# Performance work log

Hardware: AMD Instinct MI355X
Metric: run time of the kernel (lower is better)

The kernel has to match this reference:

```python
import jax, jax.numpy as jnp
import numpy as np

N, F, E, H, C, K = 20000, 256, 400000, 4, 64, 3
NEG_SLOPE = 0.2


def setup_inputs() -> dict:
    key = jax.random.key(0)
    ks = jax.random.split(key, 13)
    x = jax.random.normal(ks[0], (N, F), jnp.float32)
    edge0 = jax.random.randint(ks[1], (2, E), 0, N)
    edge1 = jax.random.randint(ks[2], (2, E), 0, N)
    edge2 = jax.random.randint(ks[3], (2, E), 0, N)
    s = 1.0 / np.sqrt(F)
    Wl = jax.random.normal(ks[4], (F, H * C), jnp.float32) * s
    bl = jax.random.normal(ks[5], (H * C,), jnp.float32) * 0.02
    Wr = jax.random.normal(ks[6], (F, H * C), jnp.float32) * s
    br = jax.random.normal(ks[7], (H * C,), jnp.float32) * 0.02
    att = jax.random.normal(ks[8], (K, H, C), jnp.float32) * (1.0 / np.sqrt(C))
    bias_out = jax.random.normal(ks[9], (K, C), jnp.float32) * 0.02
    Wg = jax.random.normal(ks[10], (F, K), jnp.float32) * s
    bg = jax.random.normal(ks[11], (K,), jnp.float32) * 0.02
    return dict(x=x, edge0=edge0, edge1=edge1, edge2=edge2, Wl=Wl, bl=bl,
                Wr=Wr, br=br, att=att, bias_out=bias_out, Wg=Wg, bg=bg)


def _gatv2_hop(xl, xr, src, dst, att_h, b_h, num_nodes):
    # xl, xr: [N, H, C] projected features (shared across hops)
    # att_h: [H, C] hop-specific attention vector; b_h: [C] hop-specific bias
    e = jax.nn.leaky_relu(xl[src] + xr[dst], NEG_SLOPE)          # [E, H, C]
    s = jnp.einsum('ehc,hc->eh', e, att_h)                       # [E, H]
    smax = jax.ops.segment_max(s, dst, num_segments=num_nodes)   # [N, H]
    ex = jnp.exp(s - smax[dst])
    denom = jax.ops.segment_sum(ex, dst, num_segments=num_nodes)
    alpha = ex / denom[dst]                                      # softmax over in-edges of dst
    msg = jax.ops.segment_sum(alpha[:, :, None] * xl[src], dst, num_segments=num_nodes)  # [N,H,C]
    return msg.mean(axis=1) + b_h                                # concat=False -> mean heads


def reference(x, edge0, edge1, edge2, Wl, bl, Wr, br, att, bias_out, Wg, bg):
    num_nodes = x.shape[0]
    heads, ch = att.shape[1], att.shape[2]
    xl = (x @ Wl + bl).reshape(num_nodes, heads, ch)
    xr = (x @ Wr + br).reshape(num_nodes, heads, ch)
    # hop 0: add self-loops (add_self_loops=True only for k == 0)
    loop = jnp.arange(num_nodes, dtype=edge0.dtype)
    src0 = jnp.concatenate([edge0[0], loop])
    dst0 = jnp.concatenate([edge0[1], loop])
    msgs = [
        _gatv2_hop(xl, xr, src0, dst0, att[0], bias_out[0], num_nodes),
        _gatv2_hop(xl, xr, edge1[0], edge1[1], att[1], bias_out[1], num_nodes),
        _gatv2_hop(xl, xr, edge2[0], edge2[1], att[2], bias_out[2], num_nodes),
    ]
    messages = jnp.stack(msgs, axis=1)                 # [N, K, C]
    logits = x @ Wg + bg                               # [N, K]
    weights = jax.nn.softmax(logits, axis=-1)
    return (messages * weights[:, :, None]).sum(axis=1)  # [N, C]
```

## Files before the change

kernel.cpp:

```cpp
#include <hip/hip_runtime.h>
#include <hip/hip_fp16.h>

#define N_NODES 20000
#define FDIM    256
#define NE      400000
#define NK      3
#define LOG2E   1.44269504088896340736f

#define TOT_EDGES (3 * NE + N_NODES)
#define NSEG      (3 * N_NODES)
#define NCHUNK    ((NSEG + 1023) / 1024)

typedef __attribute__((ext_vector_type(8))) _Float16 half8;
typedef __attribute__((ext_vector_type(4))) float f32x4;

#define PK(op, d, a, b) \
    asm("v_pk_" op "_f16 %0, %1, %2" : "=v"(d) : "v"(a), "v"(b))
#define MIX_FH(c, s, w, sel) \
    asm("v_fma_mix_f32 %0, %1, %2, %0 op_sel:[0," sel ",0] op_sel_hi:[0,1,0]" \
        : "+v"(c) : "v"(s), "v"(w))
#define MIX_HH(p, a, b, sel) \
    asm("v_fma_mix_f32 %0, %1, %2, %0 op_sel:[" sel "," sel ",0] op_sel_hi:[1,1,0]" \
        : "+v"(p) : "v"(a), "v"(b))

#define DOT2(p, e, a) { MIX_HH(p, e, a, "0"); MIX_HH(p, e, a, "1"); }

__device__ __forceinline__ float wave_sum(float x)
{
    int v = __float_as_int(x);
    int t;
    t = __builtin_amdgcn_update_dpp(0, v, 0x111, 0xf, 0xf, false);
    v = __float_as_int(__int_as_float(v) + __int_as_float(t));
    t = __builtin_amdgcn_update_dpp(0, v, 0x112, 0xf, 0xf, false);
    v = __float_as_int(__int_as_float(v) + __int_as_float(t));
    t = __builtin_amdgcn_update_dpp(0, v, 0x114, 0xf, 0xf, false);
    v = __float_as_int(__int_as_float(v) + __int_as_float(t));
    t = __builtin_amdgcn_update_dpp(0, v, 0x118, 0xf, 0xf, false);
    v = __float_as_int(__int_as_float(v) + __int_as_float(t));
    t = __builtin_amdgcn_update_dpp(0, v, 0x142, 0xa, 0xf, false);
    v = __float_as_int(__int_as_float(v) + __int_as_float(t));
    t = __builtin_amdgcn_update_dpp(0, v, 0x143, 0xc, 0xf, false);
    v = __float_as_int(__int_as_float(v) + __int_as_float(t));
    return __int_as_float(__builtin_amdgcn_readlane(v, 63));
}

__device__ __forceinline__ float rowsum16(float x)
{
    int v = __float_as_int(x);
    int t;
    t = __builtin_amdgcn_update_dpp(0, v, 0x121, 0xf, 0xf, false);
    v = __float_as_int(__int_as_float(v) + __int_as_float(t));
    t = __builtin_amdgcn_update_dpp(0, v, 0x122, 0xf, 0xf, false);
    v = __float_as_int(__int_as_float(v) + __int_as_float(t));
    t = __builtin_amdgcn_update_dpp(0, v, 0x124, 0xf, 0xf, false);
    v = __float_as_int(__int_as_float(v) + __int_as_float(t));
    t = __builtin_amdgcn_update_dpp(0, v, 0x128, 0xf, 0xf, false);
    v = __float_as_int(__int_as_float(v) + __int_as_float(t));
    return __int_as_float(v);
}

#define XCONV_V4 (N_NODES * FDIM / 4)
#define WCONV_T  (512 * 64)
#define ATT_N    (3 * 256)

__global__ __launch_bounds__(256) void conv_kernel(
    const float* __restrict__ x, const float* __restrict__ Wl,
    const float* __restrict__ Wr, const float* __restrict__ att,
    __half* __restrict__ x16, __half* __restrict__ WT16,
    __half* __restrict__ att16)
{
    int tid = blockIdx.x * blockDim.x + threadIdx.x;
    if (tid < XCONV_V4) {
        float4 v = ((const float4*)x)[tid];
        ((__half2*)x16)[tid * 2 + 0] = __floats2half2_rn(v.x, v.y);
        ((__half2*)x16)[tid * 2 + 1] = __floats2half2_rn(v.z, v.w);
    } else if (tid < XCONV_V4 + WCONV_T) {
        int q  = tid - XCONV_V4;
        int n  = q & 511;
        int k4 = (q >> 9) << 2;
        const float* Ws = (n < 256) ? Wl : Wr;
        int nn = n & 255;
        float a = Ws[(k4 + 0) * 256 + nn];
        float b = Ws[(k4 + 1) * 256 + nn];
        float c = Ws[(k4 + 2) * 256 + nn];
        float d = Ws[(k4 + 3) * 256 + nn];
        __half2* dst = (__half2*)(WT16 + (size_t)n * 256 + k4);
        dst[0] = __floats2half2_rn(a, b);
        dst[1] = __floats2half2_rn(c, d);
    } else if (tid < XCONV_V4 + WCONV_T + ATT_N) {
        int q = tid - XCONV_V4 - WCONV_T;
        att16[q] = __float2half(att[q] * LOG2E);
    }
}

__global__ __launch_bounds__(256) void gemm_mfma(
    const __half* __restrict__ x16,
    const __half* __restrict__ WT16,
    const float* __restrict__ bl, const float* __restrict__ br,
    __half* __restrict__ XL16, __half* __restrict__ XR16)
{
    __shared__ ushort As[8192];
    __shared__ ushort Bs[8192];
    char* AsB = (char*)As;
    char* BsB = (char*)Bs;

    const int t    = threadIdx.x;
    const int lane = t & 63;
    const int wid  = t >> 6;
    const int wr   = wid >> 1;
    const int wc   = wid & 1;
    const int row0 = blockIdx.x * 128;
    const int col0 = blockIdx.y * 128;
    const int sr   = t >> 1;

    f32x4 acc[4][4] = {};

    for (int k0 = 0; k0 < FDIM; k0 += 64) {
        {
            const __half* src = x16 + (size_t)(row0 + sr) * 256 + k0 + (t & 1) * 32;
            bool ok = (row0 + sr) < N_NODES;
#pragma unroll
            for (int i = 0; i < 4; ++i) {
                uint4 g = ok ? *(const uint4*)(src + i * 8)
                             : make_uint4(0, 0, 0, 0);
                *(uint4*)(AsB + sr * 128 + (((t & 1) * 4 + i) ^ (sr & 7)) * 16) = g;
            }
        }
        {
            const __half* src = WT16 + (size_t)(col0 + sr) * 256 + k0 + (t & 1) * 32;
#pragma unroll
            for (int i = 0; i < 4; ++i) {
                uint4 g = *(const uint4*)(src + i * 8);
                *(uint4*)(BsB + sr * 128 + (((t & 1) * 4 + i) ^ (sr & 7)) * 16) = g;
            }
        }
        __syncthreads();

#pragma unroll
        for (int ks = 0; ks < 2; ++ks) {
            half8 av[4], bv[4];
#pragma unroll
            for (int mi = 0; mi < 4; ++mi) {
                int arow = wr * 64 + mi * 16 + (lane & 15);
                av[mi] = *(const half8*)(AsB + arow * 128 +
                                         (((ks * 4) + (lane >> 4)) ^ (arow & 7)) * 16);
            }
#pragma unroll
            for (int ni = 0; ni < 4; ++ni) {
                int brow = wc * 64 + ni * 16 + (lane & 15);
                bv[ni] = *(const half8*)(BsB + brow * 128 +
                                         (((ks * 4) + (lane >> 4)) ^ (brow & 7)) * 16);
            }
#pragma unroll
            for (int mi = 0; mi < 4; ++mi)
#pragma unroll
                for (int ni = 0; ni < 4; ++ni)
                    acc[mi][ni] = __builtin_amdgcn_mfma_f32_16x16x32_f16(
                        av[mi], bv[ni], acc[mi][ni], 0, 0, 0);
        }
        __syncthreads();
    }

    const bool left   = (col0 < 256);
    __half* dst       = left ? XL16 : XR16;
    const float* bias = left ? bl : br;
    const int cbase   = left ? col0 : (col0 - 256);

#pragma unroll
    for (int mi = 0; mi < 4; ++mi) {
#pragma unroll
        for (int ni = 0; ni < 4; ++ni) {
            int gc = cbase + wc * 64 + ni * 16 + (lane & 15);
            float bv = bias[gc];
#pragma unroll
            for (int i = 0; i < 4; ++i) {
                int rr = row0 + wr * 64 + mi * 16 + (lane >> 4) * 4 + i;
                if (rr < N_NODES)
                    dst[(size_t)rr * 256 + gc] = __float2half(acc[mi][ni][i] + bv);
            }
        }
    }
}

__device__ __forceinline__ void decode_edge(int i, const int* e0, const int* e1,
                                            const int* e2, int& k, int& src,
                                            int& dst)
{
    if (i < NE) {
        k = 0; src = e0[i]; dst = e0[NE + i];
    } else if (i < NE + N_NODES) {
        k = 0; src = i - NE; dst = src;
    } else if (i < 2 * NE + N_NODES) {
        int j = i - (NE + N_NODES);
        k = 1; src = e1[j]; dst = e1[NE + j];
    } else {
        int j = i - (2 * NE + N_NODES);
        k = 2; src = e2[j]; dst = e2[NE + j];
    }
}

__global__ void hist_kernel(const int* __restrict__ e0,
                            const int* __restrict__ e1,
                            const int* __restrict__ e2, int* __restrict__ cnt)
{
    for (int i = blockIdx.x * blockDim.x + threadIdx.x; i < TOT_EDGES;
         i += gridDim.x * blockDim.x) {
        int k, src, dst;
        decode_edge(i, e0, e1, e2, k, src, dst);
        atomicAdd(&cnt[k * N_NODES + dst], 1);
    }
}

__global__ __launch_bounds__(1024) void scan_pass1(const int* __restrict__ cnt,
                                                   int* __restrict__ bsum)
{
    int i = blockIdx.x * 1024 + threadIdx.x;
    int v = (i < NSEG) ? cnt[i] : 0;
#pragma unroll
    for (int s = 32; s >= 1; s >>= 1) v += __shfl_xor(v, s);
    if ((threadIdx.x & 63) == 0) atomicAdd(&bsum[blockIdx.x], v);
}

__global__ __launch_bounds__(64) void scan_pass2(const int* __restrict__ bsum,
                                                 int* __restrict__ boff,
                                                 int* __restrict__ goff)
{
    int lane = threadIdx.x;
    int v = (lane < NCHUNK) ? bsum[lane] : 0;
    int incl = v;
#pragma unroll
    for (int s = 1; s < 64; s <<= 1) {
        int t = __shfl_up(incl, s);
        if (lane >= s) incl += t;
    }
    if (lane < NCHUNK) boff[lane] = incl - v;
    if (lane == NCHUNK - 1) goff[NSEG] = incl;
}

__global__ __launch_bounds__(1024) void scan_pass3(const int* __restrict__ cnt,
                                                   const int* __restrict__ boff,
                                                   int* __restrict__ goff,
                                                   int* __restrict__ cursor)
{
    __shared__ int wsum[16];
    int i    = blockIdx.x * 1024 + threadIdx.x;
    int lane = threadIdx.x & 63;
    int wid  = threadIdx.x >> 6;
    int v0 = (i < NSEG) ? cnt[i] : 0;
    int v  = v0;
#pragma unroll
    for (int s = 1; s < 64; s <<= 1) {
        int t = __shfl_up(v, s);
        if (lane >= s) v += t;
    }
    if (lane == 63) wsum[wid] = v;
    __syncthreads();
    if (wid == 0) {
        int ws = (lane < 16) ? wsum[lane] : 0;
#pragma unroll
        for (int s = 1; s < 16; s <<= 1) {
            int t = __shfl_up(ws, s);
            if (lane >= s) ws += t;
        }
        if (lane < 16) wsum[lane] = ws;
    }
    __syncthreads();
    int excl = boff[blockIdx.x] + ((wid > 0) ? wsum[wid - 1] : 0) + (v - v0);
    if (i < NSEG) { goff[i] = excl; cursor[i] = excl; }
}

__global__ void scatter_kernel(const int* __restrict__ e0,
                               const int* __restrict__ e1,
                               const int* __restrict__ e2,
                               int* __restrict__ cursor,
                               int* __restrict__ srcs)
{
    for (int i = blockIdx.x * blockDim.x + threadIdx.x; i < TOT_EDGES;
         i += gridDim.x * blockDim.x) {
        int k, src, dst;
        decode_edge(i, e0, e1, e2, k, src, dst);
        int pos = atomicAdd(&cursor[k * N_NODES + dst], 1);
        srcs[pos] = src;
    }
}

__global__ __launch_bounds__(256) void hop_kernel(
    const __half* __restrict__ XL16,
    const __half* __restrict__ XR16,
    const int* __restrict__ goff,
    const int* __restrict__ srcs,
    const __half* __restrict__ att16,
    float* __restrict__ msg)
{
    const int w    = (blockIdx.x * blockDim.x + threadIdx.x) >> 6;
    const int lane = threadIdx.x & 63;
    if (w >= NSEG) return;
    const int k = w / N_NODES;
    const int n = w - k * N_NODES;
    const int lof = lane << 2;

    const uint2 xr = *(const uint2*)(XR16 + ((size_t)n << 8) + lof);
    const uint2 at = *(const uint2*)(att16 + (k << 8) + lof);
    const unsigned K02 = 0x32663266u;

    const int jb  = goff[w];
    const int je  = goff[w + 1];
    const int cnt = je - jb;

    float den = 0.f, c0 = 0.f, c1 = 0.f, c2 = 0.f, c3 = 0.f;

    if (cnt > 0) {
        const int je1 = je - 1;
        int sv = srcs[min(jb + lane, je1)];
        uint2 w0, w1, w2, w3;
        {
            int s_;
            s_ = __builtin_amdgcn_readlane(sv, 0);
            w0 = *(const uint2*)(XL16 + ((size_t)s_ << 8) + lof);
            s_ = __builtin_amdgcn_readlane(sv, min(1, cnt - 1));
            w1 = *(const uint2*)(XL16 + ((size_t)s_ << 8) + lof);
            s_ = __builtin_amdgcn_readlane(sv, min(2, cnt - 1));
            w2 = *(const uint2*)(XL16 + ((size_t)s_ << 8) + lof);
            s_ = __builtin_amdgcn_readlane(sv, min(3, cnt - 1));
            w3 = *(const uint2*)(XL16 + ((size_t)s_ << 8) + lof);
        }

#define STEP(W, UU)                                                           \
        {                                                                     \
            unsigned z01, z23, t01, t23, e01, e23;                            \
            PK("add", z01, W.x, xr.x);                                        \
            PK("add", z23, W.y, xr.y);                                        \
            PK("mul", t01, z01, K02);                                         \
            PK("mul", t23, z23, K02);                                         \
            PK("max", e01, z01, t01);                                         \
            PK("max", e23, z23, t23);                                         \
            float p = 0.f;                                                    \
            MIX_HH(p, e01, at.x, "0");                                        \
            MIX_HH(p, e01, at.x, "1");                                        \
            MIX_HH(p, e23, at.y, "0");                                        \
            MIX_HH(p, e23, at.y, "1");                                        \
            p = rowsum16(p);                                                  \
            float ee = exp2f(p);                                              \
            ee = ((UU) < cnt) ? ee : 0.f;                                     \
            den += ee;                                                        \
            MIX_FH(c0, ee, W.x, "0");                                         \
            MIX_FH(c1, ee, W.x, "1");                                         \
            MIX_FH(c2, ee, W.y, "0");                                         \
            MIX_FH(c3, ee, W.y, "1");                                         \
            int pf = (UU) + 4;                                                \
            if (pf < cnt) {                                                   \
                if ((pf & 63) == 0) sv = srcs[min(jb + pf + lane, je1)];      \
                int s_ = __builtin_amdgcn_readlane(sv, pf & 63);              \
                W = *(const uint2*)(XL16 + ((size_t)s_ << 8) + lof);          \
            }                                                                 \
        }

        for (int u = 0; u < cnt; u += 4) {
            STEP(w0, u);
            STEP(w1, u + 1);
            STEP(w2, u + 2);
            STEP(w3, u + 3);
        }
#undef STEP
    }

    const float inv = (cnt > 0) ? (0.25f / den) : 0.f;
    float r0 = c0 * inv, r1 = c1 * inv, r2 = c2 * inv, r3 = c3 * inv;
    r0 += __shfl_xor(r0, 16); r0 += __shfl_xor(r0, 32);
    r1 += __shfl_xor(r1, 16); r1 += __shfl_xor(r1, 32);
    r2 += __shfl_xor(r2, 16); r2 += __shfl_xor(r2, 32);
    r3 += __shfl_xor(r3, 16); r3 += __shfl_xor(r3, 32);

    if (lane < 16) {
        float4 r = make_float4(r0, r1, r2, r3);
        *(float4*)(msg + ((size_t)w << 6) + (lane << 2)) = r;
    }
}

__global__ __launch_bounds__(256) void combine_kernel(
    const float* __restrict__ x, const float* __restrict__ Wg,
    const float* __restrict__ bg, const float* __restrict__ msg,
    const float* __restrict__ bias_out, float* __restrict__ out)
{
    const int n    = (blockIdx.x * blockDim.x + threadIdx.x) >> 6;
    const int lane = threadIdx.x & 63;
    if (n >= N_NODES) return;

    const float4 xv = *(const float4*)(x + (size_t)n * FDIM + (lane << 2));
    float p0 = 0.f, p1 = 0.f, p2 = 0.f;
#pragma unroll
    for (int j = 0; j < 4; ++j) {
        float xj = (&xv.x)[j];
        int f = (lane << 2) + j;
        p0 = fmaf(xj, Wg[f * 3 + 0], p0);
        p1 = fmaf(xj, Wg[f * 3 + 1], p1);
        p2 = fmaf(xj, Wg[f * 3 + 2], p2);
    }
    p0 = wave_sum(p0); p1 = wave_sum(p1); p2 = wave_sum(p2);
    float g0 = exp2f((p0 + bg[0]) * LOG2E);
    float g1 = exp2f((p1 + bg[1]) * LOG2E);
    float g2 = exp2f((p2 + bg[2]) * LOG2E);
    const float inv = 1.f / (g0 + g1 + g2);
    const float gk[3] = {g0 * inv, g1 * inv, g2 * inv};

    if (lane < 16) {
        float4 o = make_float4(0.f, 0.f, 0.f, 0.f);
#pragma unroll
        for (int k = 0; k < NK; ++k) {
            float4 m = *(const float4*)(msg +
                         (((size_t)k * N_NODES + n) << 6) + (lane << 2));
            float4 b = *(const float4*)(bias_out + (k << 6) + (lane << 2));
            float g = gk[k];
            o.x = fmaf(g, m.x + b.x, o.x);
            o.y = fmaf(g, m.y + b.y, o.y);
            o.z = fmaf(g, m.z + b.z, o.z);
            o.w = fmaf(g, m.w + b.w, o.w);
        }
        *(float4*)(out + ((size_t)n << 6) + (lane << 2)) = o;
    }
}

extern "C" void kernel_launch(void* const* d_in, const int* in_sizes, int n_in,
                              void* d_out, int out_size, void* d_ws,
                              size_t ws_size, hipStream_t stream)
{
    const float* x        = (const float*)d_in[0];
    const int*   e0       = (const int*)d_in[1];
    const int*   e1       = (const int*)d_in[2];
    const int*   e2       = (const int*)d_in[3];
    const float* Wl       = (const float*)d_in[4];
    const float* bl       = (const float*)d_in[5];
    const float* Wr       = (const float*)d_in[6];
    const float* br       = (const float*)d_in[7];
    const float* att      = (const float*)d_in[8];
    const float* bias_out = (const float*)d_in[9];
    const float* Wg       = (const float*)d_in[10];
    const float* bg       = (const float*)d_in[11];
    float* out = (float*)d_out;

    char* wsb = (char*)d_ws;
    size_t o = 0;
    __half* x16   = (__half*)(wsb + o); o += (size_t)N_NODES * 256 * sizeof(__half);
    __half* WT16  = (__half*)(wsb + o); o += (size_t)512 * 256 * sizeof(__half);
    __half* att16 = (__half*)(wsb + o); o += (size_t)ATT_N * sizeof(__half);
    __half* XL16  = (__half*)(wsb + o); o += (size_t)N_NODES * 256 * sizeof(__half);
    __half* XR16  = (__half*)(wsb + o); o += (size_t)N_NODES * 256 * sizeof(__half);
    float*  msg   = (float*)(wsb + o);  o += (size_t)NSEG * 64 * sizeof(float);
    int* cnt    = (int*)(wsb + o);   o += (size_t)NSEG * sizeof(int);
    int* bsum   = (int*)(wsb + o);   o += 64 * sizeof(int);
    int* boff   = (int*)(wsb + o);   o += 64 * sizeof(int);
    int* goff   = (int*)(wsb + o);   o += (size_t)(NSEG + 1) * sizeof(int);
    int* cursor = (int*)(wsb + o);   o += (size_t)NSEG * sizeof(int);
    int* srcs   = (int*)(wsb + o);   o += (size_t)TOT_EDGES * sizeof(int);

    hipMemsetAsync(cnt, 0, ((size_t)NSEG + 64) * sizeof(int), stream);

    int cblocks = (XCONV_V4 + WCONV_T + ATT_N + 255) / 256;
    conv_kernel<<<cblocks, 256, 0, stream>>>(x, Wl, Wr, att, x16, WT16, att16);

    dim3 ggrid((N_NODES + 127) / 128, 4);
    gemm_mfma<<<ggrid, 256, 0, stream>>>(x16, WT16, bl, br, XL16, XR16);

    int eblocks = (TOT_EDGES + 255) / 256;
    hist_kernel<<<eblocks, 256, 0, stream>>>(e0, e1, e2, cnt);
    scan_pass1<<<NCHUNK, 1024, 0, stream>>>(cnt, bsum);
    scan_pass2<<<1, 64, 0, stream>>>(bsum, boff, goff);
    scan_pass3<<<NCHUNK, 1024, 0, stream>>>(cnt, boff, goff, cursor);
    scatter_kernel<<<eblocks, 256, 0, stream>>>(e0, e1, e2, cursor, srcs);

    hop_kernel<<<(NSEG * 64 + 255) / 256, 256, 0, stream>>>(
        XL16, XR16, goff, srcs, att16, msg);

    combine_kernel<<<(N_NODES * 64 + 255) / 256, 256, 0, stream>>>(
        x, Wg, bg, msg, bias_out, out);
}
```

Baseline: 251.6 us.

## Fuse conversion, gate softmax and histogram into one prep kernel; drop scan pass2

The fp16 conversion, the degree histogram and the gating softmax now run in a single prep kernel, with the gate computed from the x values already loaded and stored to a small buffer. The separate scan_pass2 launch is removed: each scan_pass3 block sums the preceding chunk totals itself with a wave reduction and also writes the final offset. Combine now only reads the gate and uses 16 threads per node instead of a full wave, so it no longer re-reads x. This saves two launches and a full read of x, at the cost of a heavier, more branchy prep kernel.

```diff
diff --git a/kernel.cpp b/kernel.cpp
--- a/kernel.cpp
+++ b/kernel.cpp
@@ -23,7 +23,7 @@
     asm("v_fma_mix_f32 %0, %1, %2, %0 op_sel:[" sel "," sel ",0] op_sel_hi:[1,1,0]" \
         : "+v"(p) : "v"(a), "v"(b))
 
-#define DOT2(p, e, a) { MIX_HH(p, e, a, "0"); MIX_HH(p, e, a, "1"); }
+#define EXP2(x) exp2f(x)
 
 __device__ __forceinline__ float wave_sum(float x)
 {
@@ -57,129 +57,6 @@
     t = __builtin_amdgcn_update_dpp(0, v, 0x128, 0xf, 0xf, false);
     v = __float_as_int(__int_as_float(v) + __int_as_float(t));
     return __int_as_float(v);
-}
-
-#define XCONV_V4 (N_NODES * FDIM / 4)
-#define WCONV_T  (512 * 64)
-#define ATT_N    (3 * 256)
-
-__global__ __launch_bounds__(256) void conv_kernel(
-    const float* __restrict__ x, const float* __restrict__ Wl,
-    const float* __restrict__ Wr, const float* __restrict__ att,
-    __half* __restrict__ x16, __half* __restrict__ WT16,
-    __half* __restrict__ att16)
-{
-    int tid = blockIdx.x * blockDim.x + threadIdx.x;
-    if (tid < XCONV_V4) {
-        float4 v = ((const float4*)x)[tid];
-        ((__half2*)x16)[tid * 2 + 0] = __floats2half2_rn(v.x, v.y);
-        ((__half2*)x16)[tid * 2 + 1] = __floats2half2_rn(v.z, v.w);
-    } else if (tid < XCONV_V4 + WCONV_T) {
-        int q  = tid - XCONV_V4;
-        int n  = q & 511;
-        int k4 = (q >> 9) << 2;
-        const float* Ws = (n < 256) ? Wl : Wr;
-        int nn = n & 255;
-        float a = Ws[(k4 + 0) * 256 + nn];
-        float b = Ws[(k4 + 1) * 256 + nn];
-        float c = Ws[(k4 + 2) * 256 + nn];
-        float d = Ws[(k4 + 3) * 256 + nn];
-        __half2* dst = (__half2*)(WT16 + (size_t)n * 256 + k4);
-        dst[0] = __floats2half2_rn(a, b);
-        dst[1] = __floats2half2_rn(c, d);
-    } else if (tid < XCONV_V4 + WCONV_T + ATT_N) {
-        int q = tid - XCONV_V4 - WCONV_T;
-        att16[q] = __float2half(att[q] * LOG2E);
-    }
-}
-
-__global__ __launch_bounds__(256) void gemm_mfma(
-    const __half* __restrict__ x16,
-    const __half* __restrict__ WT16,
-    const float* __restrict__ bl, const float* __restrict__ br,
-    __half* __restrict__ XL16, __half* __restrict__ XR16)
-{
-    __shared__ ushort As[8192];
-    __shared__ ushort Bs[8192];
-    char* AsB = (char*)As;
-    char* BsB = (char*)Bs;
-
-    const int t    = threadIdx.x;
-    const int lane = t & 63;
-    const int wid  = t >> 6;
-    const int wr   = wid >> 1;
-    const int wc   = wid & 1;
-    const int row0 = blockIdx.x * 128;
-    const int col0 = blockIdx.y * 128;
-    const int sr   = t >> 1;
-
-    f32x4 acc[4][4] = {};
-
-    for (int k0 = 0; k0 < FDIM; k0 += 64) {
-        {
-            const __half* src = x16 + (size_t)(row0 + sr) * 256 + k0 + (t & 1) * 32;
-            bool ok = (row0 + sr) < N_NODES;
-#pragma unroll
-            for (int i = 0; i < 4; ++i) {
-                uint4 g = ok ? *(const uint4*)(src + i * 8)
-                             : make_uint4(0, 0, 0, 0);
-                *(uint4*)(AsB + sr * 128 + (((t & 1) * 4 + i) ^ (sr & 7)) * 16) = g;
-            }
-        }
-        {
-            const __half* src = WT16 + (size_t)(col0 + sr) * 256 + k0 + (t & 1) * 32;
-#pragma unroll
-            for (int i = 0; i < 4; ++i) {
-                uint4 g = *(const uint4*)(src + i * 8);
-                *(uint4*)(BsB + sr * 128 + (((t & 1) * 4 + i) ^ (sr & 7)) * 16) = g;
-            }
-        }
-        __syncthreads();
-
-#pragma unroll
-        for (int ks = 0; ks < 2; ++ks) {
-            half8 av[4], bv[4];
-#pragma unroll
-            for (int mi = 0; mi < 4; ++mi) {
-                int arow = wr * 64 + mi * 16 + (lane & 15);
-                av[mi] = *(const half8*)(AsB + arow * 128 +
-                                         (((ks * 4) + (lane >> 4)) ^ (arow & 7)) * 16);
-            }
-#pragma unroll
-            for (int ni = 0; ni < 4; ++ni) {
-                int brow = wc * 64 + ni * 16 + (lane & 15);
-                bv[ni] = *(const half8*)(BsB + brow * 128 +
-                                         (((ks * 4) + (lane >> 4)) ^ (brow & 7)) * 16);
-            }
-#pragma unroll
-            for (int mi = 0; mi < 4; ++mi)
-#pragma unroll
-                for (int ni = 0; ni < 4; ++ni)
-                    acc[mi][ni] = __builtin_amdgcn_mfma_f32_16x16x32_f16(
-                        av[mi], bv[ni], acc[mi][ni], 0, 0, 0);
-        }
-        __syncthreads();
-    }
-
-    const bool left   = (col0 < 256);
-    __half* dst       = left ? XL16 : XR16;
-    const float* bias = left ? bl : br;
-    const int cbase   = left ? col0 : (col0 - 256);
-
-#pragma unroll
-    for (int mi = 0; mi < 4; ++mi) {
-#pragma unroll
-        for (int ni = 0; ni < 4; ++ni) {
-            int gc = cbase + wc * 64 + ni * 16 + (lane & 15);
-            float bv = bias[gc];
-#pragma unroll
-            for (int i = 0; i < 4; ++i) {
-                int rr = row0 + wr * 64 + mi * 16 + (lane >> 4) * 4 + i;
-                if (rr < N_NODES)
-                    dst[(size_t)rr * 256 + gc] = __float2half(acc[mi][ni][i] + bv);
-            }
-        }
-    }
 }
 
 __device__ __forceinline__ void decode_edge(int i, const int* e0, const int* e1,
@@ -199,15 +76,164 @@
     }
 }
 
-__global__ void hist_kernel(const int* __restrict__ e0,
-                            const int* __restrict__ e1,
-                            const int* __restrict__ e2, int* __restrict__ cnt)
-{
-    for (int i = blockIdx.x * blockDim.x + threadIdx.x; i < TOT_EDGES;
-         i += gridDim.x * blockDim.x) {
-        int k, src, dst;
-        decode_edge(i, e0, e1, e2, k, src, dst);
-        atomicAdd(&cnt[k * N_NODES + dst], 1);
+#define XCONV_V4 (N_NODES * FDIM / 4)
+#define WCONV_T  (512 * 64)
+#define ATT_N    (3 * 256)
+#define CONV_T   (XCONV_V4 + WCONV_T + ATT_N)
+#define CONV_B   ((CONV_T + 255) / 256)
+#define EDGE_B   ((TOT_EDGES + 255) / 256)
+
+__global__ __launch_bounds__(256) void prep_kernel(
+    const float* __restrict__ x, const float* __restrict__ Wl,
+    const float* __restrict__ Wr, const float* __restrict__ att,
+    const float* __restrict__ Wg, const float* __restrict__ bg,
+    const int* __restrict__ e0, const int* __restrict__ e1,
+    const int* __restrict__ e2,
+    __half* __restrict__ x16, __half* __restrict__ WT16,
+    __half* __restrict__ att16, float* __restrict__ gate,
+    int* __restrict__ cnt)
+{
+    if (blockIdx.x < CONV_B) {
+        int tid = blockIdx.x * 256 + threadIdx.x;
+        if (tid < XCONV_V4) {
+            float4 v = ((const float4*)x)[tid];
+            ((__half2*)x16)[tid * 2 + 0] = __floats2half2_rn(v.x, v.y);
+            ((__half2*)x16)[tid * 2 + 1] = __floats2half2_rn(v.z, v.w);
+            const int lane = threadIdx.x & 63;
+            const int n    = tid >> 6;
+            const int f0   = lane << 2;
+            float p0 = 0.f, p1 = 0.f, p2 = 0.f;
+            const float* xe = &v.x;
+#pragma unroll
+            for (int j = 0; j < 4; ++j) {
+                float xj = xe[j];
+                p0 = fmaf(xj, Wg[(f0 + j) * 3 + 0], p0);
+                p1 = fmaf(xj, Wg[(f0 + j) * 3 + 1], p1);
+                p2 = fmaf(xj, Wg[(f0 + j) * 3 + 2], p2);
+            }
+            p0 = wave_sum(p0); p1 = wave_sum(p1); p2 = wave_sum(p2);
+            if (lane == 0) {
+                float g0 = exp2f((p0 + bg[0]) * LOG2E);
+                float g1 = exp2f((p1 + bg[1]) * LOG2E);
+                float g2 = exp2f((p2 + bg[2]) * LOG2E);
+                float inv = 1.f / (g0 + g1 + g2);
+                gate[n * 3 + 0] = g0 * inv;
+                gate[n * 3 + 1] = g1 * inv;
+                gate[n * 3 + 2] = g2 * inv;
+            }
+        } else if (tid < XCONV_V4 + WCONV_T) {
+            int q  = tid - XCONV_V4;
+            int n  = q & 511;
+            int k4 = (q >> 9) << 2;
+            const float* Ws = (n < 256) ? Wl : Wr;
+            int nn = n & 255;
+            float a = Ws[(k4 + 0) * 256 + nn];
+            float b = Ws[(k4 + 1) * 256 + nn];
+            float c = Ws[(k4 + 2) * 256 + nn];
+            float d = Ws[(k4 + 3) * 256 + nn];
+            __half2* dst = (__half2*)(WT16 + (size_t)n * 256 + k4);
+            dst[0] = __floats2half2_rn(a, b);
+            dst[1] = __floats2half2_rn(c, d);
+        } else if (tid < CONV_T) {
+            int q = tid - XCONV_V4 - WCONV_T;
+            att16[q] = __float2half(att[q] * LOG2E);
+        }
+    } else {
+        int i = (blockIdx.x - CONV_B) * 256 + threadIdx.x;
+        if (i < TOT_EDGES) {
+            int k, src, dst;
+            decode_edge(i, e0, e1, e2, k, src, dst);
+            atomicAdd(&cnt[k * N_NODES + dst], 1);
+        }
+    }
+}
+
+__global__ __launch_bounds__(256) void gemm_mfma(
+    const __half* __restrict__ x16,
+    const __half* __restrict__ WT16,
+    const float* __restrict__ bl, const float* __restrict__ br,
+    __half* __restrict__ XL16, __half* __restrict__ XR16)
+{
+    __shared__ ushort As[8192];
+    __shared__ ushort Bs[8192];
+    char* AsB = (char*)As;
+    char* BsB = (char*)Bs;
+
+    const int t    = threadIdx.x;
+    const int lane = t & 63;
+    const int wid  = t >> 6;
+    const int wr   = wid >> 1;
+    const int wc   = wid & 1;
+    const int row0 = blockIdx.x * 128;
+    const int col0 = blockIdx.y * 128;
+    const int sr   = t >> 1;
+
+    f32x4 acc[4][4] = {};
+
+    for (int k0 = 0; k0 < FDIM; k0 += 64) {
+        {
+            const __half* src = x16 + (size_t)(row0 + sr) * 256 + k0 + (t & 1) * 32;
+            bool ok = (row0 + sr) < N_NODES;
+#pragma unroll
+            for (int i = 0; i < 4; ++i) {
+                uint4 g = ok ? *(const uint4*)(src + i * 8)
+                             : make_uint4(0, 0, 0, 0);
+                *(uint4*)(AsB + sr * 128 + (((t & 1) * 4 + i) ^ (sr & 7)) * 16) = g;
+            }
+        }
+        {
+            const __half* src = WT16 + (size_t)(col0 + sr) * 256 + k0 + (t & 1) * 32;
+#pragma unroll
+            for (int i = 0; i < 4; ++i) {
+                uint4 g = *(const uint4*)(src + i * 8);
+                *(uint4*)(BsB + sr * 128 + (((t & 1) * 4 + i) ^ (sr & 7)) * 16) = g;
+            }
+        }
+        __syncthreads();
+
+#pragma unroll
+        for (int ks = 0; ks < 2; ++ks) {
+            half8 av[4], bv[4];
+#pragma unroll
+            for (int mi = 0; mi < 4; ++mi) {
+                int arow = wr * 64 + mi * 16 + (lane & 15);
+                av[mi] = *(const half8*)(AsB + arow * 128 +
+                                         (((ks * 4) + (lane >> 4)) ^ (arow & 7)) * 16);
+            }
+#pragma unroll
+            for (int ni = 0; ni < 4; ++ni) {
+                int brow = wc * 64 + ni * 16 + (lane & 15);
+                bv[ni] = *(const half8*)(BsB + brow * 128 +
+                                         (((ks * 4) + (lane >> 4)) ^ (brow & 7)) * 16);
+            }
+#pragma unroll
+            for (int mi = 0; mi < 4; ++mi)
+#pragma unroll
+                for (int ni = 0; ni < 4; ++ni)
+                    acc[mi][ni] = __builtin_amdgcn_mfma_f32_16x16x32_f16(
+                        av[mi], bv[ni], acc[mi][ni], 0, 0, 0);
+        }
+        __syncthreads();
+    }
+
+    const bool left   = (col0 < 256);
+    __half* dst       = left ? XL16 : XR16;
+    const float* bias = left ? bl : br;
+    const int cbase   = left ? col0 : (col0 - 256);
+
+#pragma unroll
+    for (int mi = 0; mi < 4; ++mi) {
+#pragma unroll
+        for (int ni = 0; ni < 4; ++ni) {
+            int gc = cbase + wc * 64 + ni * 16 + (lane & 15);
+            float bv = bias[gc];
+#pragma unroll
+            for (int i = 0; i < 4; ++i) {
+                int rr = row0 + wr * 64 + mi * 16 + (lane >> 4) * 4 + i;
+                if (rr < N_NODES)
+                    dst[(size_t)rr * 256 + gc] = __float2half(acc[mi][ni][i] + bv);
+            }
+        }
     }
 }
 
@@ -221,31 +247,22 @@
     if ((threadIdx.x & 63) == 0) atomicAdd(&bsum[blockIdx.x], v);
 }
 
-__global__ __launch_bounds__(64) void scan_pass2(const int* __restrict__ bsum,
-                                                 int* __restrict__ boff,
-                                                 int* __restrict__ goff)
-{
-    int lane = threadIdx.x;
-    int v = (lane < NCHUNK) ? bsum[lane] : 0;
-    int incl = v;
-#pragma unroll
-    for (int s = 1; s < 64; s <<= 1) {
-        int t = __shfl_up(incl, s);
-        if (lane >= s) incl += t;
-    }
-    if (lane < NCHUNK) boff[lane] = incl - v;
-    if (lane == NCHUNK - 1) goff[NSEG] = incl;
-}
-
 __global__ __launch_bounds__(1024) void scan_pass3(const int* __restrict__ cnt,
-                                                   const int* __restrict__ boff,
+                                                   const int* __restrict__ bsum,
                                                    int* __restrict__ goff,
                                                    int* __restrict__ cursor)
 {
     __shared__ int wsum[16];
-    int i    = blockIdx.x * 1024 + threadIdx.x;
-    int lane = threadIdx.x & 63;
-    int wid  = threadIdx.x >> 6;
+    __shared__ int s_boff;
+    const int lane = threadIdx.x & 63;
+    const int wid  = threadIdx.x >> 6;
+    if (wid == 0) {
+        int b = (lane < (int)blockIdx.x && lane < NCHUNK) ? bsum[lane] : 0;
+#pragma unroll
+        for (int s = 32; s >= 1; s >>= 1) b += __shfl_xor(b, s);
+        if (lane == 0) s_boff = b;
+    }
+    int i  = blockIdx.x * 1024 + threadIdx.x;
     int v0 = (i < NSEG) ? cnt[i] : 0;
     int v  = v0;
 #pragma unroll
@@ -265,8 +282,12 @@
         if (lane < 16) wsum[lane] = ws;
     }
     __syncthreads();
-    int excl = boff[blockIdx.x] + ((wid > 0) ? wsum[wid - 1] : 0) + (v - v0);
-    if (i < NSEG) { goff[i] = excl; cursor[i] = excl; }
+    int excl = s_boff + ((wid > 0) ? wsum[wid - 1] : 0) + (v - v0);
+    if (i < NSEG) {
+        goff[i]   = excl;
+        cursor[i] = excl;
+        if (i == NSEG - 1) goff[NSEG] = excl + v0;
+    }
 }
 
 __global__ void scatter_kernel(const int* __restrict__ e0,
@@ -340,7 +361,7 @@
             MIX_HH(p, e23, at.y, "0");                                        \
             MIX_HH(p, e23, at.y, "1");                                        \
             p = rowsum16(p);                                                  \
-            float ee = exp2f(p);                                              \
+            float ee = EXP2(p);                                               \
             ee = ((UU) < cnt) ? ee : 0.f;                                     \
             den += ee;                                                        \
             MIX_FH(c0, ee, W.x, "0");                                         \
@@ -378,46 +399,26 @@
 }
 
 __global__ __launch_bounds__(256) void combine_kernel(
-    const float* __restrict__ x, const float* __restrict__ Wg,
-    const float* __restrict__ bg, const float* __restrict__ msg,
+    const float* __restrict__ gate, const float* __restrict__ msg,
     const float* __restrict__ bias_out, float* __restrict__ out)
 {
-    const int n    = (blockIdx.x * blockDim.x + threadIdx.x) >> 6;
-    const int lane = threadIdx.x & 63;
+    const int n  = blockIdx.x * 16 + (threadIdx.x >> 4);
+    const int c4 = (threadIdx.x & 15) << 2;
     if (n >= N_NODES) return;
 
-    const float4 xv = *(const float4*)(x + (size_t)n * FDIM + (lane << 2));
-    float p0 = 0.f, p1 = 0.f, p2 = 0.f;
-#pragma unroll
-    for (int j = 0; j < 4; ++j) {
-        float xj = (&xv.x)[j];
-        int f = (lane << 2) + j;
-        p0 = fmaf(xj, Wg[f * 3 + 0], p0);
-        p1 = fmaf(xj, Wg[f * 3 + 1], p1);
-        p2 = fmaf(xj, Wg[f * 3 + 2], p2);
-    }
-    p0 = wave_sum(p0); p1 = wave_sum(p1); p2 = wave_sum(p2);
-    float g0 = exp2f((p0 + bg[0]) * LOG2E);
-    float g1 = exp2f((p1 + bg[1]) * LOG2E);
-    float g2 = exp2f((p2 + bg[2]) * LOG2E);
-    const float inv = 1.f / (g0 + g1 + g2);
-    const float gk[3] = {g0 * inv, g1 * inv, g2 * inv};
-
-    if (lane < 16) {
-        float4 o = make_float4(0.f, 0.f, 0.f, 0.f);
-#pragma unroll
-        for (int k = 0; k < NK; ++k) {
-            float4 m = *(const float4*)(msg +
-                         (((size_t)k * N_NODES + n) << 6) + (lane << 2));
-            float4 b = *(const float4*)(bias_out + (k << 6) + (lane << 2));
-            float g = gk[k];
-            o.x = fmaf(g, m.x + b.x, o.x);
-            o.y = fmaf(g, m.y + b.y, o.y);
-            o.z = fmaf(g, m.z + b.z, o.z);
-            o.w = fmaf(g, m.w + b.w, o.w);
-        }
-        *(float4*)(out + ((size_t)n << 6) + (lane << 2)) = o;
-    }
+    float4 o = make_float4(0.f, 0.f, 0.f, 0.f);
+#pragma unroll
+    for (int k = 0; k < NK; ++k) {
+        float g = gate[n * 3 + k];
+        float4 m = *(const float4*)(msg +
+                     (((size_t)k * N_NODES + n) << 6) + c4);
+        float4 b = *(const float4*)(bias_out + (k << 6) + c4);
+        o.x = fmaf(g, m.x + b.x, o.x);
+        o.y = fmaf(g, m.y + b.y, o.y);
+        o.z = fmaf(g, m.z + b.z, o.z);
+        o.w = fmaf(g, m.w + b.w, o.w);
+    }
+    *(float4*)(out + ((size_t)n << 6) + c4) = o;
 }
 
 extern "C" void kernel_launch(void* const* d_in, const int* in_sizes, int n_in,
@@ -448,29 +449,28 @@
     float*  msg   = (float*)(wsb + o);  o += (size_t)NSEG * 64 * sizeof(float);
     int* cnt    = (int*)(wsb + o);   o += (size_t)NSEG * sizeof(int);
     int* bsum   = (int*)(wsb + o);   o += 64 * sizeof(int);
-    int* boff   = (int*)(wsb + o);   o += 64 * sizeof(int);
     int* goff   = (int*)(wsb + o);   o += (size_t)(NSEG + 1) * sizeof(int);
     int* cursor = (int*)(wsb + o);   o += (size_t)NSEG * sizeof(int);
     int* srcs   = (int*)(wsb + o);   o += (size_t)TOT_EDGES * sizeof(int);
+    float* gate = (float*)(wsb + o); o += (size_t)N_NODES * 3 * sizeof(float);
 
     hipMemsetAsync(cnt, 0, ((size_t)NSEG + 64) * sizeof(int), stream);
 
-    int cblocks = (XCONV_V4 + WCONV_T + ATT_N + 255) / 256;
-    conv_kernel<<<cblocks, 256, 0, stream>>>(x, Wl, Wr, att, x16, WT16, att16);
+    prep_kernel<<<CONV_B + EDGE_B, 256, 0, stream>>>(
+        x, Wl, Wr, att, Wg, bg, e0, e1, e2, x16, WT16, att16, gate, cnt);
 
     dim3 ggrid((N_NODES + 127) / 128, 4);
     gemm_mfma<<<ggrid, 256, 0, stream>>>(x16, WT16, bl, br, XL16, XR16);
 
+    scan_pass1<<<NCHUNK, 1024, 0, stream>>>(cnt, bsum);
+    scan_pass3<<<NCHUNK, 1024, 0, stream>>>(cnt, bsum, goff, cursor);
+
     int eblocks = (TOT_EDGES + 255) / 256;
-    hist_kernel<<<eblocks, 256, 0, stream>>>(e0, e1, e2, cnt);
-    scan_pass1<<<NCHUNK, 1024, 0, stream>>>(cnt, bsum);
-    scan_pass2<<<1, 64, 0, stream>>>(bsum, boff, goff);
-    scan_pass3<<<NCHUNK, 1024, 0, stream>>>(cnt, boff, goff, cursor);
     scatter_kernel<<<eblocks, 256, 0, stream>>>(e0, e1, e2, cursor, srcs);
 
     hop_kernel<<<(NSEG * 64 + 255) / 256, 256, 0, stream>>>(
         XL16, XR16, goff, srcs, att16, msg);
 
-    combine_kernel<<<(N_NODES * 64 + 255) / 256, 256, 0, stream>>>(
-        x, Wg, bg, msg, bias_out, out);
-}
+    combine_kernel<<<(N_NODES + 15) / 16, 256, 0, stream>>>(
+        gate, msg, bias_out, out);
+}
```

Result: faster. 243.3 us (-3.3%).
